# Performance work log

Hardware: AMD Instinct MI355X
Metric: run time of the kernel (lower is better)

Reference implementation:

```python
import jax, jax.numpy as jnp
import numpy as np

EPS = 1e-5

def _bn_train(h, gamma, beta):
    # BatchNorm1d in training mode: batch mean and biased variance over batch dim
    mu = jnp.mean(h, axis=0)
    var = jnp.mean((h - mu) ** 2, axis=0)
    return (h - mu) * jax.lax.rsqrt(var + EPS) * gamma + beta

def setup_inputs() -> dict:
    key = jax.random.key(0)
    ks = jax.random.split(key, 12)
    B, IN, H1, H2, NC = 16384, 4096, 256, 128, 12
    x = jax.random.normal(ks[0], (B, 1, 64, 64), dtype=jnp.float32)
    y = jax.random.randint(ks[1], (B,), 0, NC, dtype=jnp.int32)
    s1 = 1.0 / np.sqrt(IN)
    W1 = jax.random.uniform(ks[2], (H1, IN), jnp.float32, -s1, s1)
    b1 = jax.random.uniform(ks[3], (H1,), jnp.float32, -s1, s1)
    g1 = jax.random.normal(ks[4], (H1,), jnp.float32) * 0.1 + 1.0
    be1 = jax.random.normal(ks[5], (H1,), jnp.float32) * 0.1
    s2 = 1.0 / np.sqrt(H1)
    W2 = jax.random.uniform(ks[6], (H2, H1), jnp.float32, -s2, s2)
    b2 = jax.random.uniform(ks[7], (H2,), jnp.float32, -s2, s2)
    g2 = jax.random.normal(ks[8], (H2,), jnp.float32) * 0.1 + 1.0
    be2 = jax.random.normal(ks[9], (H2,), jnp.float32) * 0.1
    s4 = 1.0 / np.sqrt(H2)
    W4 = jax.random.uniform(ks[10], (NC, H2), jnp.float32, -s4, s4)
    b4 = jax.random.uniform(ks[11], (NC,), jnp.float32, -s4, s4)
    return {"x": x, "W1": W1, "b1": b1, "g1": g1, "be1": be1,
            "W2": W2, "b2": b2, "g2": g2, "be2": be2,
            "W4": W4, "b4": b4, "y": y}

def reference(x, W1, b1, g1, be1, W2, b2, g2, be2, W4, b4, y):
    B = x.shape[0]
    h = x.reshape(B, -1)  # [B, 4096]
    # layer 1: binarized linear + BN(train) + hardtanh (dropout p=0 is identity)
    h = h @ jnp.sign(W1).T + jnp.sign(b1)
    h = jnp.clip(_bn_train(h, g1, be1), -1.0, 1.0)
    # layer 2
    h = h @ jnp.sign(W2).T + jnp.sign(b2)
    h = jnp.clip(_bn_train(h, g2, be2), -1.0, 1.0)
    # final float linear
    return h @ W4.T + b4  # [B, 12]
```

## Files before the change

kernel.cpp:

```cpp
#include <hip/hip_runtime.h>
#include <cstddef>

typedef __attribute__((ext_vector_type(8))) short short8;
typedef __attribute__((ext_vector_type(4))) float f4;
typedef __attribute__((ext_vector_type(4))) unsigned int u4;
typedef __attribute__((ext_vector_type(2))) unsigned int u2;

__device__ __forceinline__ unsigned int f2bf(float f){
  unsigned int u = __float_as_uint(f);
  u += 0x7fffu + ((u >> 16) & 1u);
  return u >> 16;
}
__device__ __forceinline__ float bflo(unsigned int w){ return __uint_as_float((w & 0xFFFFu) << 16); }
__device__ __forceinline__ float bfhi(unsigned int w){ return __uint_as_float(w & 0xFFFF0000u); }
__device__ __forceinline__ float fsign(float x){ return (x > 0.f) ? 1.f : ((x < 0.f) ? -1.f : 0.f); }
__device__ __forceinline__ float hclip(float x){ return fminf(1.f, fmaxf(-1.f, x)); }

#define SB0 __builtin_amdgcn_sched_barrier(0)

#define BARRIER() do { \
    SB0; \
    asm volatile("s_waitcnt lgkmcnt(0)" ::: "memory"); \
    __builtin_amdgcn_s_barrier(); \
    asm volatile("" ::: "memory"); \
    SB0; \
  } while(0)

__global__ void prep_sign_k(const float* __restrict__ W1, unsigned short* __restrict__ w1f,
                            const float* __restrict__ W2, unsigned short* __restrict__ w2s){
  int i = (blockIdx.x * blockDim.x + threadIdx.x) * 8;
  if (i < 1048576){
    int n = i >> 12, k = i & 4095;
    f4 a = *(const f4*)(W1 + i);
    f4 b = *(const f4*)(W1 + i + 4);
    u4 v;
    v.x = (unsigned)((a[0] > 0.f) ? 0x3F80u : (a[0] < 0.f ? 0xBF80u : 0u))
        | ((unsigned)((a[1] > 0.f) ? 0x3F80u : (a[1] < 0.f ? 0xBF80u : 0u)) << 16);
    v.y = (unsigned)((a[2] > 0.f) ? 0x3F80u : (a[2] < 0.f ? 0xBF80u : 0u))
        | ((unsigned)((a[3] > 0.f) ? 0x3F80u : (a[3] < 0.f ? 0xBF80u : 0u)) << 16);
    v.z = (unsigned)((b[0] > 0.f) ? 0x3F80u : (b[0] < 0.f ? 0xBF80u : 0u))
        | ((unsigned)((b[1] > 0.f) ? 0x3F80u : (b[1] < 0.f ? 0xBF80u : 0u)) << 16);
    v.w = (unsigned)((b[2] > 0.f) ? 0x3F80u : (b[2] < 0.f ? 0xBF80u : 0u))
        | ((unsigned)((b[3] > 0.f) ? 0x3F80u : (b[3] < 0.f ? 0xBF80u : 0u)) << 16);
    size_t ob = ((size_t)(k >> 5) * 256 + (size_t)n) * 64 + (size_t)((k >> 3) & 3) * 16;
    *(u4*)((char*)w1f + ob) = v;
  } else {
    int off = i - 1048576;
    if (off >= 32768) return;
    f4 a = *(const f4*)(W2 + off);
    f4 b = *(const f4*)(W2 + off + 4);
    u4 v;
    v.x = (unsigned)((a[0] > 0.f) ? 0x3F80u : (a[0] < 0.f ? 0xBF80u : 0u))
        | ((unsigned)((a[1] > 0.f) ? 0x3F80u : (a[1] < 0.f ? 0xBF80u : 0u)) << 16);
    v.y = (unsigned)((a[2] > 0.f) ? 0x3F80u : (a[2] < 0.f ? 0xBF80u : 0u))
        | ((unsigned)((a[3] > 0.f) ? 0x3F80u : (a[3] < 0.f ? 0xBF80u : 0u)) << 16);
    v.z = (unsigned)((b[0] > 0.f) ? 0x3F80u : (b[0] < 0.f ? 0xBF80u : 0u))
        | ((unsigned)((b[1] > 0.f) ? 0x3F80u : (b[1] < 0.f ? 0xBF80u : 0u)) << 16);
    v.w = (unsigned)((b[2] > 0.f) ? 0x3F80u : (b[2] < 0.f ? 0xBF80u : 0u))
        | ((unsigned)((b[3] > 0.f) ? 0x3F80u : (b[3] < 0.f ? 0xBF80u : 0u)) << 16);
    *(u4*)(w2s + off) = v;
  }
}

__global__ __launch_bounds__(512, 4) void gemm1_k(
    const float* __restrict__ x, const unsigned short* __restrict__ w1f,
    const float* __restrict__ b1, unsigned short* __restrict__ h1,
    float* __restrict__ part1s, float* __restrict__ part1q)
{
  __shared__ __align__(16) char lds[8192];
  const int tid  = threadIdx.x;
  const int lane = tid & 63;
  const int wid  = tid >> 6;
  const int cl   = lane & 15;
  const int g    = lane >> 4;
  const int row0 = blockIdx.x * 32;

  const float* xA = x + (size_t)(row0 + (tid >> 4)) * 4096 + (tid & 15) * 4;
  const int aw = (tid >> 4) * 128 + (((tid & 15) * 8) ^ (((tid >> 4) & 7) << 4));

  const char* w1p = (const char*)w1f;
  const int bof0 = (wid * 32 +  0 + cl) * 64 + g * 16;
  const int bof1 = (wid * 32 + 16 + cl) * 64 + g * 16;

  int afo[2][2];
  #pragma unroll
  for (int fm = 0; fm < 2; fm++){
    int m = fm * 16 + cl;
    afo[fm][0] = m * 128 + ((     g * 16) ^ ((m & 7) << 4));
    afo[fm][1] = m * 128 + ((64 + g * 16) ^ ((m & 7) << 4));
  }

  f4 acc[2][2];
  const f4 z = {0.f, 0.f, 0.f, 0.f};
  acc[0][0] = z; acc[0][1] = z; acc[1][0] = z; acc[1][1] = z;

  f4 rA0, rA1, rA2, rA3;
  short8 B00, B01, B10, B11;

#define ISSUEA(S, K) do { rA##S = *(const f4*)(xA + (size_t)(K) * 64); } while(0)

#define ISSUEB(K) do { \
    const char* _p = w1p + (size_t)(K) * 32768; \
    B00 = *(const short8*)(_p +         bof0); \
    B01 = *(const short8*)(_p + 16384 + bof0); \
    B10 = *(const short8*)(_p +         bof1); \
    B11 = *(const short8*)(_p + 16384 + bof1); \
  } while(0)

#define PACKA(S, AB) do { \
    u2 _v; \
    _v.x = f2bf(rA##S[0]) | (f2bf(rA##S[1]) << 16); \
    _v.y = f2bf(rA##S[2]) | (f2bf(rA##S[3]) << 16); \
    *(u2*)(lds + (AB) * 4096 + aw) = _v; \
  } while(0)

#define COMPUTE(KI) do { \
    const char* _ab = lds + ((KI) & 1) * 4096; \
    short8 _af00 = *(const short8*)(_ab + afo[0][0]); \
    short8 _af01 = *(const short8*)(_ab + afo[0][1]); \
    short8 _af10 = *(const short8*)(_ab + afo[1][0]); \
    short8 _af11 = *(const short8*)(_ab + afo[1][1]); \
    __builtin_amdgcn_s_setprio(1); \
    acc[0][0] = __builtin_amdgcn_mfma_f32_16x16x32_bf16(_af00, B00, acc[0][0], 0, 0, 0); \
    acc[0][1] = __builtin_amdgcn_mfma_f32_16x16x32_bf16(_af00, B10, acc[0][1], 0, 0, 0); \
    acc[1][0] = __builtin_amdgcn_mfma_f32_16x16x32_bf16(_af10, B00, acc[1][0], 0, 0, 0); \
    acc[1][1] = __builtin_amdgcn_mfma_f32_16x16x32_bf16(_af10, B10, acc[1][1], 0, 0, 0); \
    acc[0][0] = __builtin_amdgcn_mfma_f32_16x16x32_bf16(_af01, B01, acc[0][0], 0, 0, 0); \
    acc[0][1] = __builtin_amdgcn_mfma_f32_16x16x32_bf16(_af01, B11, acc[0][1], 0, 0, 0); \
    acc[1][0] = __builtin_amdgcn_mfma_f32_16x16x32_bf16(_af01, B01, acc[1][0], 0, 0, 0); \
    acc[1][1] = __builtin_amdgcn_mfma_f32_16x16x32_bf16(_af11, B11, acc[1][1], 0, 0, 0); \
  } while(0)
#undef COMPUTE
#define COMPUTE(KI) do { \
    const char* _ab = lds + ((KI) & 1) * 4096; \
    short8 _af00 = *(const short8*)(_ab + afo[0][0]); \
    short8 _af01 = *(const short8*)(_ab + afo[0][1]); \
    short8 _af10 = *(const short8*)(_ab + afo[1][0]); \
    short8 _af11 = *(const short8*)(_ab + afo[1][1]); \
    __builtin_amdgcn_s_setprio(1); \
    acc[0][0] = __builtin_amdgcn_mfma_f32_16x16x32_bf16(_af00, B00, acc[0][0], 0, 0, 0); \
    acc[0][1] = __builtin_amdgcn_mfma_f32_16x16x32_bf16(_af00, B10, acc[0][1], 0, 0, 0); \
    acc[1][0] = __builtin_amdgcn_mfma_f32_16x16x32_bf16(_af10, B00, acc[1][0], 0, 0, 0); \
    acc[1][1] = __builtin_amdgcn_mfma_f32_16x16x32_bf16(_af10, B10, acc[1][1], 0, 0, 0); \
    acc[0][0] = __builtin_amdgcn_mfma_f32_16x16x32_bf16(_af01, B01, acc[0][0], 0, 0, 0); \
    acc[0][1] = __builtin_amdgcn_mfma_f32_16x16x32_bf16(_af01, B11, acc[0][1], 0, 0, 0); \
    acc[1][0] = __builtin_amdgcn_mfma_f32_16x16x32_bf16(_af11, B01, acc[1][0], 0, 0, 0); \
    acc[1][1] = __builtin_amdgcn_mfma_f32_16x16x32_bf16(_af11, B11, acc[1][1], 0, 0, 0); \
    __builtin_amdgcn_s_setprio(0); \
  } while(0)

#define STEP(K, AS3, AP1) do { \
    COMPUTE(K); \
    ISSUEB(((K) + 1 < 64) ? (K) + 1 : 63); \
    ISSUEA(AS3, ((K) + 3 < 64) ? (K) + 3 : 63); \
    SB0; \
    if ((K) < 63) PACKA(AP1, ((K) + 1) & 1); \
    BARRIER(); \
  } while(0)

  ISSUEB(0);
  ISSUEA(0, 0); ISSUEA(1, 1); ISSUEA(2, 2);
  SB0;
  PACKA(0, 0);
  BARRIER();

  #pragma unroll 1
  for (int kk = 0; kk < 64; kk += 4){
    STEP(kk + 0, 3, 1);
    STEP(kk + 1, 0, 2);
    STEP(kk + 2, 1, 3);
    STEP(kk + 3, 2, 0);
  }
  asm volatile("s_waitcnt vmcnt(0)" ::: "memory");

#undef STEP
#undef COMPUTE
#undef PACKA
#undef ISSUEB
#undef ISSUEA

  #pragma unroll
  for (int fn = 0; fn < 2; fn++){
    int c = wid * 32 + fn * 16 + cl;
    float sb = fsign(b1[c]);
    float s = 0.f, q = 0.f;
    #pragma unroll
    for (int fm = 0; fm < 2; fm++){
      int rbase = row0 + fm * 16 + g * 4;
      #pragma unroll
      for (int i = 0; i < 4; i++){
        float v = acc[fm][fn][i] + sb;
        h1[(size_t)(rbase + i) * 256 + c] = (unsigned short)f2bf(v);
        s += v; q += v * v;
      }
    }
    s += __shfl_xor(s, 16, 64); s += __shfl_xor(s, 32, 64);
    q += __shfl_xor(q, 16, 64); q += __shfl_xor(q, 32, 64);
    if (g == 0){
      part1s[(size_t)c * 512 + blockIdx.x] = s;
      part1q[(size_t)c * 512 + blockIdx.x] = q;
    }
  }
}

template<int COLS, int NBLK>
__global__ __launch_bounds__(64) void params_k(
    const float* __restrict__ ps, const float* __restrict__ pq,
    const float* __restrict__ g, const float* __restrict__ be,
    float* __restrict__ ab){
  int j = blockIdx.x * 64 + threadIdx.x;
  const f4* vs = (const f4*)(ps + (size_t)j * NBLK);
  const f4* vq = (const f4*)(pq + (size_t)j * NBLK);
  f4 s4 = {0,0,0,0}, q4 = {0,0,0,0};
  #pragma unroll 8
  for (int b = 0; b < NBLK/4; b++){ s4 += vs[b]; q4 += vq[b]; }
  float s = s4[0]+s4[1]+s4[2]+s4[3];
  float q = q4[0]+q4[1]+q4[2]+q4[3];
  float mu  = s * (1.f/16384.f);
  float var = q * (1.f/16384.f) - mu*mu;
  float a   = g[j] * rsqrtf(var + 1e-5f);
  ab[j] = a;
  ab[COLS + j] = be[j] - mu*a;
}

__global__ __launch_bounds__(512) void gemm2_k(
    const unsigned short* __restrict__ h1, const unsigned short* __restrict__ w2s,
    const float* __restrict__ b2, const float* __restrict__ ab1,
    unsigned short* __restrict__ h2, float* __restrict__ part2s, float* __restrict__ part2q)
{
  __shared__ __align__(16) char lds[32768];
  __shared__ __align__(16) float a1l[256];
  __shared__ __align__(16) float c1l[256];
  const int tid  = threadIdx.x;
  const int lane = tid & 63;
  const int wid  = tid >> 6;
  const int cl   = lane & 15;
  const int g    = lane >> 4;
  const int klo  = g * 8;
  const int row0 = blockIdx.x * 64;

  if (tid < 256) a1l[tid] = ab1[tid];
  else           c1l[tid - 256] = ab1[tid];

  const int am  = tid >> 3;
  const int ak0 = (tid & 7) * 8;
  const unsigned short* hA = h1 + (size_t)(row0 + am) * 256 + ak0;
  const int aw = ((am * 128) + (ak0 * 2)) ^ ((am & 7) << 4);
  const unsigned short* wbase = w2s + (size_t)(wid * 16 + cl) * 256 + klo;

  u4 q0 = *(const u4*)(hA);
  u4 q1 = *(const u4*)(hA + 64);
  u4 q2 = *(const u4*)(hA + 128);
  u4 q3 = *(const u4*)(hA + 192);
  short8 Bq0, Bq1, Br0, Br1;
  Bq0 = *(const short8*)(wbase);
  Bq1 = *(const short8*)(wbase + 32);

  BARRIER();

#define TRW(KB, RAW) do { \
    f4 _a0 = *(const f4*)(&a1l[(KB)*64 + ak0]); \
    f4 _a1 = *(const f4*)(&a1l[(KB)*64 + ak0 + 4]); \
    f4 _c0 = *(const f4*)(&c1l[(KB)*64 + ak0]); \
    f4 _c1 = *(const f4*)(&c1l[(KB)*64 + ak0 + 4]); \
    float _t0 = hclip(_a0[0]*bflo(RAW.x) + _c0[0]); \
    float _t1 = hclip(_a0[1]*bfhi(RAW.x) + _c0[1]); \
    float _t2 = hclip(_a0[2]*bflo(RAW.y) + _c0[2]); \
    float _t3 = hclip(_a0[3]*bfhi(RAW.y) + _c0[3]); \
    float _t4 = hclip(_a1[0]*bflo(RAW.z) + _c1[0]); \
    float _t5 = hclip(_a1[1]*bfhi(RAW.z) + _c1[1]); \
    float _t6 = hclip(_a1[2]*bflo(RAW.w) + _c1[2]); \
    float _t7 = hclip(_a1[3]*bfhi(RAW.w) + _c1[3]); \
    u4 _v; \
    _v.x = f2bf(_t0) | (f2bf(_t1) << 16); \
    _v.y = f2bf(_t2) | (f2bf(_t3) << 16); \
    _v.z = f2bf(_t4) | (f2bf(_t5) << 16); \
    _v.w = f2bf(_t6) | (f2bf(_t7) << 16); \
    *(u4*)(lds + (KB)*8192 + aw) = _v; \
  } while(0)

  TRW(0, q0); TRW(1, q1); TRW(2, q2); TRW(3, q3);
#undef TRW
  BARRIER();

  f4 acc[4];
  const f4 z = {0.f, 0.f, 0.f, 0.f};
  #pragma unroll
  for (int i = 0; i < 4; i++) acc[i] = z;

#define LOADB2(P, KB) do { \
    B##P##0 = *(const short8*)(wbase + (KB)*64); \
    B##P##1 = *(const short8*)(wbase + (KB)*64 + 32); \
  } while(0)

#define COMP2(BASE, P) do { \
    const char* _ab = (const char*)(BASE); \
    short8 _af[4][2]; \
    _Pragma("unroll") \
    for (int fm = 0; fm < 4; fm++){ \
      int _m = fm*16 + cl; \
      _af[fm][0] = *(const short8*)(_ab + ((_m*128 + klo*2) ^ ((_m & 7) << 4))); \
      _af[fm][1] = *(const short8*)(_ab + ((_m*128 + (32 + klo)*2) ^ ((_m & 7) << 4))); \
    } \
    _Pragma("unroll") \
    for (int fm = 0; fm < 4; fm++){ \
      acc[fm] = __builtin_amdgcn_mfma_f32_16x16x32_bf16(_af[fm][0], B##P##0, acc[fm], 0, 0, 0); \
      acc[fm] = __builtin_amdgcn_mfma_f32_16x16x32_bf16(_af[fm][1], B##P##1, acc[fm], 0, 0, 0); \
    } \
  } while(0)

  LOADB2(r, 1);
  COMP2(lds,         q);
  LOADB2(q, 2);
  COMP2(lds +  8192, r);
  LOADB2(r, 3);
  COMP2(lds + 16384, q);
  COMP2(lds + 24576, r);
#undef COMP2
#undef LOADB2

  {
    int c = wid*16 + cl;
    float sb = fsign(b2[c]);
    float s = 0.f, q = 0.f;
    #pragma unroll
    for (int fm = 0; fm < 4; fm++){
      int rbase = row0 + fm*16 + g*4;
      #pragma unroll
      for (int i = 0; i < 4; i++){
        float v = acc[fm][i] + sb;
        h2[(size_t)(rbase + i)*128 + c] = (unsigned short)f2bf(v);
        s += v; q += v*v;
      }
    }
    s += __shfl_xor(s, 16, 64); s += __shfl_xor(s, 32, 64);
    q += __shfl_xor(q, 16, 64); q += __shfl_xor(q, 32, 64);
    if (g == 0){
      part2s[c*256 + blockIdx.x] = s;
      part2q[c*256 + blockIdx.x] = q;
    }
  }
}

__global__ __launch_bounds__(128) void final_k(
    const unsigned short* __restrict__ h2,
    const float* __restrict__ part2s, const float* __restrict__ part2q,
    const float* __restrict__ g2, const float* __restrict__ be2,
    const float* __restrict__ W4, const float* __restrict__ b4,
    float* __restrict__ out)
{
  __shared__ __align__(16) float W4l[12*128];
  __shared__ __align__(16) float a2l[128];
  __shared__ __align__(16) float c2l[128];
  const int t = threadIdx.x;
  #pragma unroll
  for (int i = 0; i < 3; i++)
    *(f4*)&W4l[(i*128 + t)*4] = *(const f4*)(W4 + (i*128 + t)*4);
  {
    const f4* vs = (const f4*)(part2s + t*256);
    const f4* vq = (const f4*)(part2q + t*256);
    f4 s4 = {0,0,0,0}, q4 = {0,0,0,0};
    #pragma unroll 8
    for (int b = 0; b < 64; b++){ s4 += vs[b]; q4 += vq[b]; }
    float s = s4[0]+s4[1]+s4[2]+s4[3];
    float q = q4[0]+q4[1]+q4[2]+q4[3];
    float mu  = s * (1.f/16384.f);
    float var = q * (1.f/16384.f) - mu*mu;
    float a   = g2[t] * rsqrtf(var + 1e-5f);
    a2l[t] = a;
    c2l[t] = be2[t] - mu*a;
  }
  __syncthreads();

  const int r = blockIdx.x * 128 + t;
  const u4* hp = (const u4*)(h2 + (size_t)r * 128);
  u4 hv0 = hp[0], hv1 = hp[1], hv2 = hp[2],  hv3 = hp[3];
  u4 hv4 = hp[4], hv5 = hp[5], hv6 = hp[6],  hv7 = hp[7];
  u4 hv8 = hp[8], hv9 = hp[9], hv10 = hp[10], hv11 = hp[11];
  u4 hv12 = hp[12], hv13 = hp[13], hv14 = hp[14], hv15 = hp[15];

  float acc[12];
  #pragma unroll
  for (int o = 0; o < 12; o++) acc[o] = b4[o];

#define FPROC(HV, J) do { \
    f4 a0 = *(const f4*)&a2l[(J)*8];     f4 a1 = *(const f4*)&a2l[(J)*8 + 4]; \
    f4 c0 = *(const f4*)&c2l[(J)*8];     f4 c1 = *(const f4*)&c2l[(J)*8 + 4]; \
    float tt0 = hclip(a0[0]*bflo(HV.x) + c0[0]); \
    float tt1 = hclip(a0[1]*bfhi(HV.x) + c0[1]); \
    float tt2 = hclip(a0[2]*bflo(HV.y) + c0[2]); \
    float tt3 = hclip(a0[3]*bfhi(HV.y) + c0[3]); \
    float tt4 = hclip(a1[0]*bflo(HV.z) + c1[0]); \
    float tt5 = hclip(a1[1]*bfhi(HV.z) + c1[1]); \
    float tt6 = hclip(a1[2]*bflo(HV.w) + c1[2]); \
    float tt7 = hclip(a1[3]*bfhi(HV.w) + c1[3]); \
    _Pragma("unroll") \
    for (int o = 0; o < 12; o++){ \
      f4 w0 = *(const f4*)&W4l[o*128 + (J)*8]; \
      f4 w1 = *(const f4*)&W4l[o*128 + (J)*8 + 4]; \
      acc[o] += tt0*w0[0] + tt1*w0[1] + tt2*w0[2] + tt3*w0[3] \
              + tt4*w1[0] + tt5*w1[1] + tt6*w1[2] + tt7*w1[3]; \
    } \
  } while(0)

  FPROC(hv0, 0);  FPROC(hv1, 1);  FPROC(hv2, 2);   FPROC(hv3, 3);
  FPROC(hv4, 4);  FPROC(hv5, 5);  FPROC(hv6, 6);   FPROC(hv7, 7);
  FPROC(hv8, 8);  FPROC(hv9, 9);  FPROC(hv10, 10); FPROC(hv11, 11);
  FPROC(hv12, 12); FPROC(hv13, 13); FPROC(hv14, 14); FPROC(hv15, 15);
#undef FPROC

  #pragma unroll
  for (int o = 0; o < 12; o++) out[(size_t)r*12 + o] = acc[o];
}

extern "C" void kernel_launch(void* const* d_in, const int* in_sizes, int n_in,
                              void* d_out, int out_size, void* d_ws, size_t ws_size,
                              hipStream_t stream)
{
  const float* x   = (const float*)d_in[0];
  const float* W1  = (const float*)d_in[1];
  const float* b1  = (const float*)d_in[2];
  const float* g1  = (const float*)d_in[3];
  const float* be1 = (const float*)d_in[4];
  const float* W2  = (const float*)d_in[5];
  const float* b2  = (const float*)d_in[6];
  const float* g2  = (const float*)d_in[7];
  const float* be2 = (const float*)d_in[8];
  const float* W4  = (const float*)d_in[9];
  const float* b4  = (const float*)d_in[10];
  float* out = (float*)d_out;

  char* ws = (char*)d_ws;
  unsigned short* h1     = (unsigned short*)(ws);
  unsigned short* h2     = (unsigned short*)(ws + 8388608);
  unsigned short* w1f    = (unsigned short*)(ws + 12582912);
  unsigned short* w2s    = (unsigned short*)(ws + 14680064);
  float*          part1s = (float*)(ws + 14745600);
  float*          part1q = (float*)(ws + 15269888);
  float*          part2s = (float*)(ws + 15794176);
  float*          part2q = (float*)(ws + 15925248);
  float*          ab1    = (float*)(ws + 16056320);

  prep_sign_k<<<528, 256, 0, stream>>>(W1, w1f, W2, w2s);
  gemm1_k<<<512, 512, 0, stream>>>(x, w1f, b1, h1, part1s, part1q);
  params_k<256, 512><<<4, 64, 0, stream>>>(part1s, part1q, g1, be1, ab1);
  gemm2_k<<<256, 512, 0, stream>>>(h1, w2s, b2, ab1, h2, part2s, part2q);
  final_k<<<128, 128, 0, stream>>>(h2, part2s, part2q, g2, be2, W4, b4, out);
}
```

Baseline: 143.3 us.

## Load A fragments directly into registers in gemm1 and enlarge per-wave tile

Rewrites gemm1 so each wave loads its x rows straight from global memory into MFMA fragment layout and converts them to bf16 in registers, dropping the LDS staging buffer and all per-step barriers. Blocks now cover 64 rows with a 2x4 wave grid, so each wave computes a 32x64 tile and W1 fragments are reused across more rows. The grid is halved, launch bounds drop to 2 blocks per SM, and the partial-stat indexing is adjusted for two row-halves per block. The trade-off is more register pressure, lower occupancy, and x loads that are no longer shared between waves, with 4 waves reading the same x rows.

Measured after the change: 232.1 us. 61.9% more time.

```diff
diff --git a/kernel.cpp b/kernel.cpp
--- a/kernel.cpp
+++ b/kernel.cpp
@@ -4,7 +4,6 @@
 typedef __attribute__((ext_vector_type(8))) short short8;
 typedef __attribute__((ext_vector_type(4))) float f4;
 typedef __attribute__((ext_vector_type(4))) unsigned int u4;
-typedef __attribute__((ext_vector_type(2))) unsigned int u2;
 
 __device__ __forceinline__ unsigned int f2bf(float f){
   unsigned int u = __float_as_uint(f);
@@ -62,131 +61,134 @@
   }
 }
 
-__global__ __launch_bounds__(512, 4) void gemm1_k(
+__global__ __launch_bounds__(512, 2) void gemm1_k(
     const float* __restrict__ x, const unsigned short* __restrict__ w1f,
     const float* __restrict__ b1, unsigned short* __restrict__ h1,
     float* __restrict__ part1s, float* __restrict__ part1q)
 {
-  __shared__ __align__(16) char lds[8192];
   const int tid  = threadIdx.x;
   const int lane = tid & 63;
   const int wid  = tid >> 6;
+  const int wm   = wid >> 2;
+  const int wn   = wid & 3;
   const int cl   = lane & 15;
   const int g    = lane >> 4;
-  const int row0 = blockIdx.x * 32;
-
-  const float* xA = x + (size_t)(row0 + (tid >> 4)) * 4096 + (tid & 15) * 4;
-  const int aw = (tid >> 4) * 128 + (((tid & 15) * 8) ^ (((tid >> 4) & 7) << 4));
+  const int row0 = blockIdx.x * 64;
+
+  const char* xr0 = (const char*)(x + (size_t)(row0 + wm * 32 +  0 + cl) * 4096) + g * 32;
+  const char* xr1 = (const char*)(x + (size_t)(row0 + wm * 32 + 16 + cl) * 4096) + g * 32;
 
   const char* w1p = (const char*)w1f;
-  const int bof0 = (wid * 32 +  0 + cl) * 64 + g * 16;
-  const int bof1 = (wid * 32 + 16 + cl) * 64 + g * 16;
-
-  int afo[2][2];
-  #pragma unroll
-  for (int fm = 0; fm < 2; fm++){
-    int m = fm * 16 + cl;
-    afo[fm][0] = m * 128 + ((     g * 16) ^ ((m & 7) << 4));
-    afo[fm][1] = m * 128 + ((64 + g * 16) ^ ((m & 7) << 4));
-  }
-
-  f4 acc[2][2];
+  const int bof0 = (wn * 64 +  0 + cl) * 64 + g * 16;
+  const int bof1 = (wn * 64 + 16 + cl) * 64 + g * 16;
+  const int bof2 = (wn * 64 + 32 + cl) * 64 + g * 16;
+  const int bof3 = (wn * 64 + 48 + cl) * 64 + g * 16;
+
+  f4 acc[2][4];
   const f4 z = {0.f, 0.f, 0.f, 0.f};
-  acc[0][0] = z; acc[0][1] = z; acc[1][0] = z; acc[1][1] = z;
-
-  f4 rA0, rA1, rA2, rA3;
-  short8 B00, B01, B10, B11;
-
-#define ISSUEA(S, K) do { rA##S = *(const f4*)(xA + (size_t)(K) * 64); } while(0)
+  #pragma unroll
+  for (int i = 0; i < 2; i++)
+    #pragma unroll
+    for (int j = 0; j < 4; j++) acc[i][j] = z;
+
+  f4 r0_00a, r0_00b, r0_01a, r0_01b, r0_10a, r0_10b, r0_11a, r0_11b;
+  f4 r1_00a, r1_00b, r1_01a, r1_01b, r1_10a, r1_10b, r1_11a, r1_11b;
+  short8 a00, a01, a10, a11;
+  short8 b00, b01, b10, b11, b20, b21, b30, b31;
+
+#define ISSUEA(P, K) do { \
+    size_t _o = (size_t)(K) * 256; \
+    r##P##_00a = *(const f4*)(xr0 + _o);       r##P##_00b = *(const f4*)(xr0 + _o + 16); \
+    r##P##_01a = *(const f4*)(xr0 + _o + 128); r##P##_01b = *(const f4*)(xr0 + _o + 144); \
+    r##P##_10a = *(const f4*)(xr1 + _o);       r##P##_10b = *(const f4*)(xr1 + _o + 16); \
+    r##P##_11a = *(const f4*)(xr1 + _o + 128); r##P##_11b = *(const f4*)(xr1 + _o + 144); \
+  } while(0)
 
 #define ISSUEB(K) do { \
     const char* _p = w1p + (size_t)(K) * 32768; \
-    B00 = *(const short8*)(_p +         bof0); \
-    B01 = *(const short8*)(_p + 16384 + bof0); \
-    B10 = *(const short8*)(_p +         bof1); \
-    B11 = *(const short8*)(_p + 16384 + bof1); \
-  } while(0)
-
-#define PACKA(S, AB) do { \
-    u2 _v; \
-    _v.x = f2bf(rA##S[0]) | (f2bf(rA##S[1]) << 16); \
-    _v.y = f2bf(rA##S[2]) | (f2bf(rA##S[3]) << 16); \
-    *(u2*)(lds + (AB) * 4096 + aw) = _v; \
-  } while(0)
-
-#define COMPUTE(KI) do { \
-    const char* _ab = lds + ((KI) & 1) * 4096; \
-    short8 _af00 = *(const short8*)(_ab + afo[0][0]); \
-    short8 _af01 = *(const short8*)(_ab + afo[0][1]); \
-    short8 _af10 = *(const short8*)(_ab + afo[1][0]); \
-    short8 _af11 = *(const short8*)(_ab + afo[1][1]); \
+    b00 = *(const short8*)(_p +         bof0);  b01 = *(const short8*)(_p + 16384 + bof0); \
+    b10 = *(const short8*)(_p +         bof1);  b11 = *(const short8*)(_p + 16384 + bof1); \
+    b20 = *(const short8*)(_p +         bof2);  b21 = *(const short8*)(_p + 16384 + bof2); \
+    b30 = *(const short8*)(_p +         bof3);  b31 = *(const short8*)(_p + 16384 + bof3); \
+  } while(0)
+
+#define CVT1(DST, RA, RB) do { \
+    u4 _pk; \
+    _pk.x = f2bf(RA[0]) | (f2bf(RA[1]) << 16); \
+    _pk.y = f2bf(RA[2]) | (f2bf(RA[3]) << 16); \
+    _pk.z = f2bf(RB[0]) | (f2bf(RB[1]) << 16); \
+    _pk.w = f2bf(RB[2]) | (f2bf(RB[3]) << 16); \
+    DST = *(short8*)&_pk; \
+  } while(0)
+
+#define CONVA(P) do { \
+    CVT1(a00, r##P##_00a, r##P##_00b); \
+    CVT1(a01, r##P##_01a, r##P##_01b); \
+    CVT1(a10, r##P##_10a, r##P##_10b); \
+    CVT1(a11, r##P##_11a, r##P##_11b); \
+  } while(0)
+
+#define MFMA16() do { \
     __builtin_amdgcn_s_setprio(1); \
-    acc[0][0] = __builtin_amdgcn_mfma_f32_16x16x32_bf16(_af00, B00, acc[0][0], 0, 0, 0); \
-    acc[0][1] = __builtin_amdgcn_mfma_f32_16x16x32_bf16(_af00, B10, acc[0][1], 0, 0, 0); \
-    acc[1][0] = __builtin_amdgcn_mfma_f32_16x16x32_bf16(_af10, B00, acc[1][0], 0, 0, 0); \
-    acc[1][1] = __builtin_amdgcn_mfma_f32_16x16x32_bf16(_af10, B10, acc[1][1], 0, 0, 0); \
-    acc[0][0] = __builtin_amdgcn_mfma_f32_16x16x32_bf16(_af01, B01, acc[0][0], 0, 0, 0); \
-    acc[0][1] = __builtin_amdgcn_mfma_f32_16x16x32_bf16(_af01, B11, acc[0][1], 0, 0, 0); \
-    acc[1][0] = __builtin_amdgcn_mfma_f32_16x16x32_bf16(_af01, B01, acc[1][0], 0, 0, 0); \
-    acc[1][1] = __builtin_amdgcn_mfma_f32_16x16x32_bf16(_af11, B11, acc[1][1], 0, 0, 0); \
-  } while(0)
-#undef COMPUTE
-#define COMPUTE(KI) do { \
-    const char* _ab = lds + ((KI) & 1) * 4096; \
-    short8 _af00 = *(const short8*)(_ab + afo[0][0]); \
-    short8 _af01 = *(const short8*)(_ab + afo[0][1]); \
-    short8 _af10 = *(const short8*)(_ab + afo[1][0]); \
-    short8 _af11 = *(const short8*)(_ab + afo[1][1]); \
-    __builtin_amdgcn_s_setprio(1); \
-    acc[0][0] = __builtin_amdgcn_mfma_f32_16x16x32_bf16(_af00, B00, acc[0][0], 0, 0, 0); \
-    acc[0][1] = __builtin_amdgcn_mfma_f32_16x16x32_bf16(_af00, B10, acc[0][1], 0, 0, 0); \
-    acc[1][0] = __builtin_amdgcn_mfma_f32_16x16x32_bf16(_af10, B00, acc[1][0], 0, 0, 0); \
-    acc[1][1] = __builtin_amdgcn_mfma_f32_16x16x32_bf16(_af10, B10, acc[1][1], 0, 0, 0); \
-    acc[0][0] = __builtin_amdgcn_mfma_f32_16x16x32_bf16(_af01, B01, acc[0][0], 0, 0, 0); \
-    acc[0][1] = __builtin_amdgcn_mfma_f32_16x16x32_bf16(_af01, B11, acc[0][1], 0, 0, 0); \
-    acc[1][0] = __builtin_amdgcn_mfma_f32_16x16x32_bf16(_af11, B01, acc[1][0], 0, 0, 0); \
-    acc[1][1] = __builtin_amdgcn_mfma_f32_16x16x32_bf16(_af11, B11, acc[1][1], 0, 0, 0); \
+    acc[0][0] = __builtin_amdgcn_mfma_f32_16x16x32_bf16(a00, b00, acc[0][0], 0, 0, 0); \
+    acc[0][1] = __builtin_amdgcn_mfma_f32_16x16x32_bf16(a00, b10, acc[0][1], 0, 0, 0); \
+    acc[0][2] = __builtin_amdgcn_mfma_f32_16x16x32_bf16(a00, b20, acc[0][2], 0, 0, 0); \
+    acc[0][3] = __builtin_amdgcn_mfma_f32_16x16x32_bf16(a00, b30, acc[0][3], 0, 0, 0); \
+    acc[1][0] = __builtin_amdgcn_mfma_f32_16x16x32_bf16(a10, b00, acc[1][0], 0, 0, 0); \
+    acc[1][1] = __builtin_amdgcn_mfma_f32_16x16x32_bf16(a10, b10, acc[1][1], 0, 0, 0); \
+    acc[1][2] = __builtin_amdgcn_mfma_f32_16x16x32_bf16(a10, b20, acc[1][2], 0, 0, 0); \
+    acc[1][3] = __builtin_amdgcn_mfma_f32_16x16x32_bf16(a10, b30, acc[1][3], 0, 0, 0); \
+    acc[0][0] = __builtin_amdgcn_mfma_f32_16x16x32_bf16(a01, b01, acc[0][0], 0, 0, 0); \
+    acc[0][1] = __builtin_amdgcn_mfma_f32_16x16x32_bf16(a01, b11, acc[0][1], 0, 0, 0); \
+    acc[0][2] = __builtin_amdgcn_mfma_f32_16x16x32_bf16(a01, b21, acc[0][2], 0, 0, 0); \
+    acc[0][3] = __builtin_amdgcn_mfma_f32_16x16x32_bf16(a01, b31, acc[0][3], 0, 0, 0); \
+    acc[1][0] = __builtin_amdgcn_mfma_f32_16x16x32_bf16(a11, b01, acc[1][0], 0, 0, 0); \
+    acc[1][1] = __builtin_amdgcn_mfma_f32_16x16x32_bf16(a11, b11, acc[1][1], 0, 0, 0); \
+    acc[1][2] = __builtin_amdgcn_mfma_f32_16x16x32_bf16(a11, b21, acc[1][2], 0, 0, 0); \
+    acc[1][3] = __builtin_amdgcn_mfma_f32_16x16x32_bf16(a11, b31, acc[1][3], 0, 0, 0); \
     __builtin_amdgcn_s_setprio(0); \
   } while(0)
 
-#define STEP(K, AS3, AP1) do { \
-    COMPUTE(K); \
+#define STEP(K, P1) do { \
+    MFMA16(); \
+    SB0; \
     ISSUEB(((K) + 1 < 64) ? (K) + 1 : 63); \
-    ISSUEA(AS3, ((K) + 3 < 64) ? (K) + 3 : 63); \
-    SB0; \
-    if ((K) < 63) PACKA(AP1, ((K) + 1) & 1); \
-    BARRIER(); \
-  } while(0)
-
+    SB0; \
+    CONVA(P1); \
+    SB0; \
+    ISSUEA(P1, ((K) + 3 < 64) ? (K) + 3 : 63); \
+    SB0; \
+  } while(0)
+
+  ISSUEA(0, 0);
   ISSUEB(0);
-  ISSUEA(0, 0); ISSUEA(1, 1); ISSUEA(2, 2);
   SB0;
-  PACKA(0, 0);
-  BARRIER();
-
-  #pragma unroll 1
-  for (int kk = 0; kk < 64; kk += 4){
-    STEP(kk + 0, 3, 1);
-    STEP(kk + 1, 0, 2);
-    STEP(kk + 2, 1, 3);
-    STEP(kk + 3, 2, 0);
+  CONVA(0);
+  ISSUEA(1, 1);
+  ISSUEA(0, 2);
+  SB0;
+
+  for (int k = 0; k < 64; k += 2){
+    STEP(k,     1);
+    STEP(k + 1, 0);
   }
   asm volatile("s_waitcnt vmcnt(0)" ::: "memory");
 
 #undef STEP
-#undef COMPUTE
-#undef PACKA
+#undef MFMA16
+#undef CONVA
+#undef CVT1
 #undef ISSUEB
 #undef ISSUEA
 
   #pragma unroll
-  for (int fn = 0; fn < 2; fn++){
-    int c = wid * 32 + fn * 16 + cl;
+  for (int fn = 0; fn < 4; fn++){
+    int c = wn * 64 + fn * 16 + cl;
     float sb = fsign(b1[c]);
     float s = 0.f, q = 0.f;
     #pragma unroll
     for (int fm = 0; fm < 2; fm++){
-      int rbase = row0 + fm * 16 + g * 4;
+      int rbase = row0 + wm * 32 + fm * 16 + g * 4;
       #pragma unroll
       for (int i = 0; i < 4; i++){
         float v = acc[fm][fn][i] + sb;
@@ -197,8 +199,8 @@
     s += __shfl_xor(s, 16, 64); s += __shfl_xor(s, 32, 64);
     q += __shfl_xor(q, 16, 64); q += __shfl_xor(q, 32, 64);
     if (g == 0){
-      part1s[(size_t)c * 512 + blockIdx.x] = s;
-      part1q[(size_t)c * 512 + blockIdx.x] = q;
+      part1s[(size_t)c * 512 + blockIdx.x * 2 + wm] = s;
+      part1q[(size_t)c * 512 + blockIdx.x * 2 + wm] = q;
     }
   }
 }
@@ -442,7 +444,7 @@
   float*          ab1    = (float*)(ws + 16056320);
 
   prep_sign_k<<<528, 256, 0, stream>>>(W1, w1f, W2, w2s);
-  gemm1_k<<<512, 512, 0, stream>>>(x, w1f, b1, h1, part1s, part1q);
+  gemm1_k<<<256, 512, 0, stream>>>(x, w1f, b1, h1, part1s, part1q);
   params_k<256, 512><<<4, 64, 0, stream>>>(part1s, part1q, g1, be1, ab1);
   gemm2_k<<<256, 512, 0, stream>>>(h1, w2s, b2, ab1, h2, part2s, part2q);
   final_k<<<128, 128, 0, stream>>>(h2, part2s, part2q, g2, be2, W4, b4, out);
```
